# Performance work log

Measured on AMD Instinct MI355X. Metric: run time of the kernel, lower is better.

The kernel has to match this reference:

```python
import jax, jax.numpy as jnp
import numpy as np

N = 50000      # nodes
E = 800000     # edges
F = 128        # node feature dim (= output_size, residual)
H = 128        # hidden_size

def _uniform_fan_avg(key, shape):
    # VarianceScaling(scale=1.0, mode='fan_avg', distribution='uniform')
    fan_avg = (shape[0] + shape[1]) / 2.0
    limit = np.sqrt(3.0 / fan_avg)
    return jax.random.uniform(key, shape, jnp.float32, -limit, limit)

def setup_inputs() -> dict:
    key = jax.random.key(0)
    ks = jax.random.split(key, 16)
    h = jax.random.normal(ks[0], (N, F), jnp.float32)
    pos = jax.random.normal(ks[1], (N, 3), jnp.float32)
    senders = jax.random.randint(ks[2], (E,), 0, N, jnp.int32)
    receivers = jax.random.randint(ks[3], (E,), 0, N, jnp.int32)
    # edge_mlp: Linear(2F+1 -> H) silu, Linear(H -> H) silu (activate_final=True)
    eW1 = _uniform_fan_avg(ks[4], (2 * F + 1, H)); eb1 = jnp.zeros((H,), jnp.float32)
    eW2 = _uniform_fan_avg(ks[5], (H, H)); eb2 = jnp.zeros((H,), jnp.float32)
    # node_mlp: Linear(F+H -> H) silu, Linear(H -> F) (no final act)
    nW1 = _uniform_fan_avg(ks[6], (F + H, H)); nb1 = jnp.zeros((H,), jnp.float32)
    nW2 = _uniform_fan_avg(ks[7], (H, F)); nb2 = jnp.zeros((F,), jnp.float32)
    # pos_correction_mlp: Linear(H -> H) silu, Linear(H -> 1, no bias, UniformScaling(dt))
    pW1 = _uniform_fan_avg(ks[8], (H, H)); pb1 = jnp.zeros((H,), jnp.float32)
    dt = 0.001
    pW2 = jax.random.uniform(ks[9], (H, 1), jnp.float32, -dt, dt) * np.sqrt(3.0)
    return {"h": h, "pos": pos, "senders": senders, "receivers": receivers,
            "eW1": eW1, "eb1": eb1, "eW2": eW2, "eb2": eb2,
            "nW1": nW1, "nb1": nb1, "nW2": nW2, "nb2": nb2,
            "pW1": pW1, "pb1": pb1, "pW2": pW2}

def reference(h, pos, senders, receivers,
              eW1, eb1, eW2, eb2,
              nW1, nb1, nW2, nb2,
              pW1, pb1, pW2):
    n = h.shape[0]
    # _coord2radial (normalize=False)
    coord_diff = pos[senders] - pos[receivers]            # [E,3]
    radial = jnp.sum(coord_diff ** 2, axis=1, keepdims=True)  # [E,1]
    # edge update (_message): concat(h[senders], h[receivers], radial) -> edge_mlp
    msg_in = jnp.concatenate([h[senders], h[receivers], radial], axis=-1)  # [E,2F+1]
    msg = jax.nn.silu(msg_in @ eW1 + eb1)
    msg = jax.nn.silu(msg @ eW2 + eb2)                    # [E,H]
    # node update (_update): aggregate messages at receivers, node_mlp, residual
    agg = jax.ops.segment_sum(msg, receivers, num_segments=n)  # [N,H]
    x = jnp.concatenate([h, agg], axis=-1)                # [N,F+H]
    x = jax.nn.silu(x @ nW1 + nb1)
    x = x @ nW2 + nb2                                     # [N,F]
    h_new = h + x                                         # residual
    # position update (_pos_update)
    pc = jax.nn.silu(msg @ pW1 + pb1) @ pW2               # [E,1]
    trans = jnp.clip(coord_diff * pc, -100, 100)          # [E,3]
    pos_new = pos + jax.ops.segment_sum(trans, senders, num_segments=n)
    return h_new, pos_new
```

## Files before the change

### kernel.cpp

```cpp
#include <hip/hip_runtime.h>
#include <hip/hip_bf16.h>

#define NNODES 50000
#define NEDGES 800000
#define EB 1024
#define SCAN_BLOCKS 196
#define TRN_BLOCKS 448

typedef short bf16x8 __attribute__((ext_vector_type(8)));
typedef float f32x4 __attribute__((ext_vector_type(4)));
typedef unsigned short u16;
typedef unsigned int u32;

__device__ __forceinline__ u16 f2bf(float f) {
    __hip_bfloat16 b = __float2bfloat16(f);
    return *reinterpret_cast<u16*>(&b);
}
__device__ __forceinline__ float bf2f(u16 v) {
    u32 u = ((u32)v) << 16;
    return __uint_as_float(u);
}
__device__ __forceinline__ u32 pack2(float a, float b) {
    __hip_bfloat162 t = __float22bfloat162_rn(float2{a, b});
    return *reinterpret_cast<u32*>(&t);
}
__device__ __forceinline__ float fast_silu(float x) {
    float e = __builtin_amdgcn_exp2f(-1.442695040888963f * x);
    return x * __builtin_amdgcn_rcpf(1.0f + e);
}
__device__ __forceinline__ bf16x8 ld8(const u16* p) {
    return *(const bf16x8*)p;
}
__device__ __forceinline__ f32x4 mfma16(bf16x8 a, bf16x8 b, f32x4 c) {
    return __builtin_amdgcn_mfma_f32_16x16x32_bf16(a, b, c, 0, 0, 0);
}

__global__ void prep_kernel(const float* __restrict__ eW1, const float* __restrict__ eW2,
                            const float* __restrict__ pW1, const float* __restrict__ nW1,
                            const float* __restrict__ nW2,
                            u16* __restrict__ eW1T, u16* __restrict__ eW2T,
                            u16* __restrict__ pW1T, u16* __restrict__ nW1T,
                            u16* __restrict__ nW2T,
                            const int* __restrict__ rcv, int* __restrict__ counts) {
    int b = blockIdx.x;
    if (b < TRN_BLOCKS) {
        int i = b * 256 + threadIdx.x;
        const float* src; u16* dst; int K;
        if (i < 32768)      { src = eW1; dst = eW1T; K = 256; }
        else if (i < 49152) { src = eW2; dst = eW2T; K = 128; i -= 32768; }
        else if (i < 65536) { src = pW1; dst = pW1T; K = 128; i -= 49152; }
        else if (i < 98304) { src = nW1; dst = nW1T; K = 256; i -= 65536; }
        else                { src = nW2; dst = nW2T; K = 128; i -= 98304; }
        int n = i / K, k = i - n * K;
        dst[i] = f2bf(src[k * 128 + n]);
    } else {
        int e = (b - TRN_BLOCKS) * 256 + threadIdx.x;
        if (e < NEDGES) atomicAdd(&counts[rcv[e]], 1);
    }
}

__global__ __launch_bounds__(256) void gemm_p(
    const float* __restrict__ h, const u16* __restrict__ eW1T,
    const u16* __restrict__ nW1T, const float* __restrict__ eb1,
    u16* __restrict__ P)
{
    const int tid  = threadIdx.x;
    const int w    = tid >> 6;
    const int lane = tid & 63;
    const int m    = lane & 15;
    const int quad = lane >> 4;
    const int ksub = quad * 8;

    bf16x8 bw[4][6];
    float bias[6];
    #pragma unroll
    for (int cc = 0; cc < 6; cc++) {
        int C = 96 * w + 16 * cc + m;
        const u16* bp;
        if (C < 128)      { bp = eW1T + C * 256;               bias[cc] = 0.5f * eb1[C]; }
        else if (C < 256) { bp = eW1T + (C - 128) * 256 + 128; bias[cc] = 0.5f * eb1[C - 128]; }
        else              { bp = nW1T + (C - 256) * 256;       bias[cc] = 0.f; }
        #pragma unroll
        for (int t = 0; t < 4; t++) bw[t][cc] = ld8(bp + t * 32 + ksub);
    }
    const int base = blockIdx.x * 64;
    #pragma unroll
    for (int mt = 0; mt < 4; mt++) {
        int nm = base + mt * 16 + m;
        if (nm >= NNODES) nm = NNODES - 1;
        bf16x8 afr[4];
        #pragma unroll
        for (int t = 0; t < 4; t++) {
            const float* ap = h + (size_t)nm * 128 + t * 32 + ksub;
            f32x4 lo = *(const f32x4*)ap;
            f32x4 hi = *(const f32x4*)(ap + 4);
            #pragma unroll
            for (int j = 0; j < 4; j++) {
                afr[t][j]     = (short)f2bf(lo[j]);
                afr[t][4 + j] = (short)f2bf(hi[j]);
            }
        }
        f32x4 acc[6];
        #pragma unroll
        for (int cc = 0; cc < 6; cc++) acc[cc] = (f32x4){0,0,0,0};
        #pragma unroll
        for (int t = 0; t < 4; t++)
            #pragma unroll
            for (int cc = 0; cc < 6; cc++)
                acc[cc] = mfma16(afr[t], bw[t][cc], acc[cc]);
        #pragma unroll
        for (int cc = 0; cc < 6; cc++) {
            int C = 96 * w + 16 * cc + m;
            #pragma unroll
            for (int r = 0; r < 4; r++) {
                int nr = base + mt * 16 + quad * 4 + r;
                if (nr < NNODES) P[(size_t)nr * 384 + C] = f2bf(acc[cc][r] + bias[cc]);
            }
        }
    }
}

__global__ void scan1(const int* __restrict__ counts, int* __restrict__ excl,
                      int* __restrict__ blkSum) {
    __shared__ int tmp[256];
    int tx = threadIdx.x;
    int i = blockIdx.x * 256 + tx;
    int v = (i < NNODES) ? counts[i] : 0;
    tmp[tx] = v;
    __syncthreads();
    for (int off = 1; off < 256; off <<= 1) {
        int t = (tx >= off) ? tmp[tx - off] : 0;
        __syncthreads();
        tmp[tx] += t;
        __syncthreads();
    }
    if (i < NNODES) excl[i] = tmp[tx] - v;
    if (tx == 255) blkSum[blockIdx.x] = tmp[255];
}
__global__ void scan2(const int* __restrict__ blkSum, int* __restrict__ blkOff) {
    __shared__ int tmp[256];
    int tx = threadIdx.x;
    int v = (tx < SCAN_BLOCKS) ? blkSum[tx] : 0;
    tmp[tx] = v;
    __syncthreads();
    for (int off = 1; off < 256; off <<= 1) {
        int t = (tx >= off) ? tmp[tx - off] : 0;
        __syncthreads();
        tmp[tx] += t;
        __syncthreads();
    }
    if (tx < SCAN_BLOCKS) blkOff[tx] = tmp[tx] - v;
}
__global__ void scan3(const int* __restrict__ excl, const int* __restrict__ blkOff,
                      int* __restrict__ cursor) {
    int i = blockIdx.x * 256 + threadIdx.x;
    if (i < NNODES) cursor[i] = excl[i] + blkOff[blockIdx.x];
}
__global__ void scatter_kernel(const int* __restrict__ rcv, int* __restrict__ cursor,
                               int* __restrict__ perm) {
    int e = blockIdx.x * 256 + threadIdx.x;
    if (e < NEDGES) {
        int p = atomicAdd(&cursor[rcv[e]], 1);
        perm[p] = e;
    }
}

struct __align__(16) EdgeLds {
    u16   m1[64 * 136];
    u16   msg[64 * 136];
    float diff[64][4];
    float pcpart[4][64];
    float wlast[128];
    float radial[64];
    int   sndloc[64];
    int   rcvloc[64];
};

__global__ __launch_bounds__(256, 4) void edge_kernel(
    const u16* __restrict__ P, const float* __restrict__ pos,
    const int* __restrict__ snd, const int* __restrict__ rcv,
    const int* __restrict__ perm,
    const float* __restrict__ eW1last,
    const u16* __restrict__ eW2T, const float* __restrict__ eb2,
    const u16* __restrict__ pW1T, const float* __restrict__ pb1,
    const float* __restrict__ pW2,
    float* __restrict__ agg, float* __restrict__ posacc)
{
    __shared__ EdgeLds S;
    const int tid  = threadIdx.x;
    const int w    = tid >> 6;
    const int lane = tid & 63;
    const int m    = lane & 15;
    const int quad = lane >> 4;
    const int ksub = quad * 8;

    bf16x8 bw2[4][2], bp1[4][2];
    float b2v[2], pb1v[2], pw2v[2];
    #pragma unroll
    for (int cc = 0; cc < 2; cc++) {
        int col = (2 * w + cc) * 16 + m;
        #pragma unroll
        for (int t = 0; t < 4; t++) {
            bw2[t][cc] = ld8(eW2T + col * 128 + t * 32 + ksub);
            bp1[t][cc] = ld8(pW1T + col * 128 + t * 32 + ksub);
        }
        b2v[cc]  = eb2[col];
        pb1v[cc] = pb1[col];
        pw2v[cc] = pW2[col];
    }
    if (tid < 128) S.wlast[tid] = eW1last[tid];

    for (int base = blockIdx.x * 64; base < NEDGES; base += gridDim.x * 64) {
        __syncthreads();
        const int e = lane;
        int eg = perm[base + e];
        int s = snd[eg], r = rcv[eg];
        if (tid < 64) {
            S.sndloc[tid] = s; S.rcvloc[tid] = r;
            float rad = 0.f;
            #pragma unroll
            for (int c = 0; c < 3; c++) {
                float d = pos[s * 3 + c] - pos[r * 3 + c];
                S.diff[tid][c] = d;
                rad += d * d;
            }
            S.radial[tid] = rad;
        }
        __syncthreads();
        {
            float rad = S.radial[e];
            const u16* pa = P + (size_t)s * 384 + w * 32;
            const u16* pb = P + (size_t)r * 384 + 128 + w * 32;
            const int sw = e >> 3;
            #pragma unroll
            for (int k = 0; k < 4; k++) {
                bf16x8 va = ld8(pa + k * 8);
                bf16x8 vb = ld8(pb + k * 8);
                u32 pk[4];
                #pragma unroll
                for (int jj = 0; jj < 4; jj++) {
                    int col = w * 32 + k * 8 + jj * 2;
                    float2 wl = *(const float2*)&S.wlast[col];
                    float v0 = bf2f((u16)va[jj * 2])     + bf2f((u16)vb[jj * 2])     + rad * wl.x;
                    float v1 = bf2f((u16)va[jj * 2 + 1]) + bf2f((u16)vb[jj * 2 + 1]) + rad * wl.y;
                    pk[jj] = pack2(fast_silu(v0), fast_silu(v1));
                }
                int chunk = (w * 4 + k) ^ sw;
                *(uint4*)&S.m1[e * 136 + chunk * 8] =
                    make_uint4(pk[0], pk[1], pk[2], pk[3]);
            }
        }
        __syncthreads();
        #pragma unroll
        for (int mt = 0; mt < 4; mt++) {
            const int rs = mt * 2 + (m >> 3);
            const int row = mt * 16 + m;
            f32x4 acc0 = (f32x4){0,0,0,0}, acc1 = (f32x4){0,0,0,0};
            #pragma unroll
            for (int t = 0; t < 4; t++) {
                bf16x8 a = *(const bf16x8*)&S.m1[row * 136 + ((t * 4 + quad) ^ rs) * 8];
                acc0 = mfma16(a, bw2[t][0], acc0);
                acc1 = mfma16(a, bw2[t][1], acc1);
            }
            #pragma unroll
            for (int cc = 0; cc < 2; cc++) {
                f32x4 acc = cc ? acc1 : acc0;
                int col = (2 * w + cc) * 16 + m;
                #pragma unroll
                for (int rr = 0; rr < 4; rr++) {
                    int orow = mt * 16 + quad * 4 + rr;
                    S.msg[orow * 136 + col] = f2bf(fast_silu(acc[rr] + b2v[cc]));
                }
            }
        }
        __syncthreads();
        #pragma unroll
        for (int mt = 0; mt < 4; mt++) {
            f32x4 acc0 = (f32x4){0,0,0,0}, acc1 = (f32x4){0,0,0,0};
            #pragma unroll
            for (int t = 0; t < 4; t++) {
                bf16x8 a = *(const bf16x8*)&S.msg[(mt * 16 + m) * 136 + t * 32 + ksub];
                acc0 = mfma16(a, bp1[t][0], acc0);
                acc1 = mfma16(a, bp1[t][1], acc1);
            }
            float p4[4];
            #pragma unroll
            for (int rr = 0; rr < 4; rr++)
                p4[rr] = fast_silu(acc0[rr] + pb1v[0]) * pw2v[0]
                       + fast_silu(acc1[rr] + pb1v[1]) * pw2v[1];
            #pragma unroll
            for (int mask = 1; mask < 16; mask <<= 1) {
                #pragma unroll
                for (int rr = 0; rr < 4; rr++) p4[rr] += __shfl_xor(p4[rr], mask);
            }
            if (m == 0) {
                #pragma unroll
                for (int rr = 0; rr < 4; rr++)
                    S.pcpart[w][mt * 16 + quad * 4 + rr] = p4[rr];
            }
        }
        {
            int half = tid >> 7, col = tid & 127;
            int r0 = half * 32;
            float a = 0.f;
            int cur = S.rcvloc[r0];
            for (int rr = r0; rr < r0 + 32; ++rr) {
                int rc = S.rcvloc[rr];
                if (rc != cur) {
                    atomicAdd(&agg[(size_t)cur * 128 + col], a);
                    a = 0.f; cur = rc;
                }
                a += bf2f(S.msg[rr * 136 + col]);
            }
            atomicAdd(&agg[(size_t)cur * 128 + col], a);
        }
        __syncthreads();
        if (tid < 192) {
            int ee = tid / 3, c = tid - ee * 3;
            float pc = S.pcpart[0][ee] + S.pcpart[1][ee] + S.pcpart[2][ee] + S.pcpart[3][ee];
            float tr = S.diff[ee][c] * pc;
            tr = fminf(fmaxf(tr, -100.f), 100.f);
            atomicAdd(&posacc[S.sndloc[ee] * 3 + c], tr);
        }
    }
}

__global__ __launch_bounds__(256, 4) void node_kernel(
    const u16* __restrict__ P, const float* __restrict__ h,
    const float* __restrict__ agg,
    const u16* __restrict__ nW1T, const float* __restrict__ nb1,
    const u16* __restrict__ nW2T, const float* __restrict__ nb2,
    const float* __restrict__ pos, const float* __restrict__ posacc,
    float* __restrict__ out)
{
    __shared__ alignas(16) u16 m1[64 * 136];
    const int tid  = threadIdx.x;
    const int w    = tid >> 6;
    const int lane = tid & 63;
    const int m    = lane & 15;
    const int quad = lane >> 4;
    const int ksub = quad * 8;

    bf16x8 bw1[4][2], bw2[4][2];
    float b1v[2], b2v[2];
    #pragma unroll
    for (int cc = 0; cc < 2; cc++) {
        int col = (2 * w + cc) * 16 + m;
        #pragma unroll
        for (int t = 0; t < 4; t++) {
            bw1[t][cc] = ld8(nW1T + col * 256 + 128 + t * 32 + ksub);
            bw2[t][cc] = ld8(nW2T + col * 128 + t * 32 + ksub);
        }
        b1v[cc] = nb1[col];
        b2v[cc] = nb2[col];
    }
    const int base = blockIdx.x * 64;
    #pragma unroll
    for (int mt = 0; mt < 4; mt++) {
        int nm = base + mt * 16 + m;
        if (nm >= NNODES) nm = NNODES - 1;
        f32x4 acc0 = (f32x4){0,0,0,0}, acc1 = (f32x4){0,0,0,0};
        #pragma unroll
        for (int t = 0; t < 4; t++) {
            const float* ap = agg + (size_t)nm * 128 + t * 32 + ksub;
            f32x4 lo = *(const f32x4*)ap;
            f32x4 hi = *(const f32x4*)(ap + 4);
            bf16x8 a;
            #pragma unroll
            for (int j = 0; j < 4; j++) {
                a[j]     = (short)f2bf(lo[j]);
                a[4 + j] = (short)f2bf(hi[j]);
            }
            acc0 = mfma16(a, bw1[t][0], acc0);
            acc1 = mfma16(a, bw1[t][1], acc1);
        }
        #pragma unroll
        for (int cc = 0; cc < 2; cc++) {
            f32x4 acc = cc ? acc1 : acc0;
            int col = (2 * w + cc) * 16 + m;
            #pragma unroll
            for (int rr = 0; rr < 4; rr++) {
                int row = mt * 16 + quad * 4 + rr;
                int nrc = base + row; if (nrc >= NNODES) nrc = NNODES - 1;
                float v = acc[rr] + bf2f(P[(size_t)nrc * 384 + 256 + col]) + b1v[cc];
                m1[row * 136 + col] = f2bf(fast_silu(v));
            }
        }
    }
    __syncthreads();
    #pragma unroll
    for (int mt = 0; mt < 4; mt++) {
        f32x4 acc0 = (f32x4){0,0,0,0}, acc1 = (f32x4){0,0,0,0};
        #pragma unroll
        for (int t = 0; t < 4; t++) {
            bf16x8 a = *(const bf16x8*)&m1[(mt * 16 + m) * 136 + t * 32 + ksub];
            acc0 = mfma16(a, bw2[t][0], acc0);
            acc1 = mfma16(a, bw2[t][1], acc1);
        }
        #pragma unroll
        for (int cc = 0; cc < 2; cc++) {
            f32x4 acc = cc ? acc1 : acc0;
            int col = (2 * w + cc) * 16 + m;
            #pragma unroll
            for (int rr = 0; rr < 4; rr++) {
                int nr = base + mt * 16 + quad * 4 + rr;
                if (nr < NNODES)
                    out[(size_t)nr * 128 + col] = acc[rr] + b2v[cc] + h[(size_t)nr * 128 + col];
            }
        }
    }
    if (tid < 192) {
        int i = blockIdx.x * 192 + tid;
        if (i < NNODES * 3) out[NNODES * 128 + i] = pos[i] + posacc[i];
    }
}

extern "C" void kernel_launch(void* const* d_in, const int* in_sizes, int n_in,
                              void* d_out, int out_size, void* d_ws, size_t ws_size,
                              hipStream_t stream) {
    (void)in_sizes; (void)n_in; (void)out_size; (void)ws_size;
    const float* h   = (const float*)d_in[0];
    const float* pos = (const float*)d_in[1];
    const int*   snd = (const int*)d_in[2];
    const int*   rcv = (const int*)d_in[3];
    const float* eW1 = (const float*)d_in[4];
    const float* eb1 = (const float*)d_in[5];
    const float* eW2 = (const float*)d_in[6];
    const float* eb2 = (const float*)d_in[7];
    const float* nW1 = (const float*)d_in[8];
    const float* nb1 = (const float*)d_in[9];
    const float* nW2 = (const float*)d_in[10];
    const float* nb2 = (const float*)d_in[11];
    const float* pW1 = (const float*)d_in[12];
    const float* pb1 = (const float*)d_in[13];
    const float* pW2 = (const float*)d_in[14];
    float* out = (float*)d_out;

    float* agg    = (float*)d_ws;
    float* posacc = agg + (size_t)NNODES * 128;
    u16* P    = (u16*)(posacc + (size_t)NNODES * 3);
    u16* eW1T = P + (size_t)NNODES * 384;
    u16* eW2T = eW1T + 128 * 256;
    u16* pW1T = eW2T + 128 * 128;
    u16* nW1T = pW1T + 128 * 128;
    u16* nW2T = nW1T + 128 * 256;
    int* counts = (int*)(nW2T + 128 * 128);
    int* excl   = counts + 50048;
    int* blkSum = excl + 50048;
    int* blkOff = blkSum + 256;
    int* cursor = blkOff + 256;
    int* perm   = cursor + 50048;

    hipMemsetAsync(agg, 0, (size_t)NNODES * 131 * sizeof(float), stream);
    hipMemsetAsync(counts, 0, 50048 * sizeof(int), stream);

    prep_kernel<<<TRN_BLOCKS + (NEDGES + 255) / 256, 256, 0, stream>>>(
        eW1, eW2, pW1, nW1, nW2, eW1T, eW2T, pW1T, nW1T, nW2T, rcv, counts);

    gemm_p<<<(NNODES + 63) / 64, 256, 0, stream>>>(h, eW1T, nW1T, eb1, P);

    scan1<<<SCAN_BLOCKS, 256, 0, stream>>>(counts, excl, blkSum);
    scan2<<<1, 256, 0, stream>>>(blkSum, blkOff);
    scan3<<<SCAN_BLOCKS, 256, 0, stream>>>(excl, blkOff, cursor);
    scatter_kernel<<<(NEDGES + 255) / 256, 256, 0, stream>>>(rcv, cursor, perm);

    edge_kernel<<<EB, 256, 0, stream>>>(
        P, pos, snd, rcv, perm,
        eW1 + 256 * 128,
        eW2T, eb2, pW1T, pb1, pW2,
        agg, posacc);

    node_kernel<<<(NNODES + 63) / 64, 256, 0, stream>>>(
        P, h, agg, nW1T, nb1, nW2T, nb2, pos, posacc, out);
}
```

Before: 445.2 us.

## Software-pipeline edge gathers across iterations and use ballot bitmap for segment boundaries

Edge indices, positions and projected node features for the next 64-edge tile are prefetched into registers while the current tile's MFMA stages run, hiding gather latency. One block barrier is removed by computing the radial term in registers, and the others become lightweight LDS-only barriers. Segment boundaries for the receiver-sorted aggregation come from a wave ballot bitmap rather than a per-row compare loop. In exchange, register pressure rises under a 4-blocks-per-SIMD launch bound, which could cause spills. The custom barrier waits only on LDS counters, so it relies on global loads never being read through shared memory.

Measured after the change: 553.0 us. 1.24x slower.

```diff
diff --git a/kernel.cpp b/kernel.cpp
--- a/kernel.cpp
+++ b/kernel.cpp
@@ -33,6 +33,9 @@
 }
 __device__ __forceinline__ f32x4 mfma16(bf16x8 a, bf16x8 b, f32x4 c) {
     return __builtin_amdgcn_mfma_f32_16x16x32_bf16(a, b, c, 0, 0, 0);
+}
+__device__ __forceinline__ void bar_lds() {
+    asm volatile("s_waitcnt lgkmcnt(0)\n\ts_barrier" ::: "memory");
 }
 
 __global__ void prep_kernel(const float* __restrict__ eW1, const float* __restrict__ eW2,
@@ -171,9 +174,9 @@
     float diff[64][4];
     float pcpart[4][64];
     float wlast[128];
-    float radial[64];
     int   sndloc[64];
     int   rcvloc[64];
+    unsigned long long bmap;
 };
 
 __global__ __launch_bounds__(256, 4) void edge_kernel(
@@ -210,32 +213,53 @@
     }
     if (tid < 128) S.wlast[tid] = eW1last[tid];
 
-    for (int base = blockIdx.x * 64; base < NEDGES; base += gridDim.x * 64) {
-        __syncthreads();
-        const int e = lane;
-        int eg = perm[base + e];
-        int s = snd[eg], r = rcv[eg];
+    const int stride = gridDim.x * 64;
+
+    int s_n, r_n;
+    float ps_n[3], pr_n[3];
+    bf16x8 pa_n[4], pb_n[4];
+    {
+        int eg = perm[blockIdx.x * 64 + lane];
+        s_n = snd[eg]; r_n = rcv[eg];
+        #pragma unroll
+        for (int c = 0; c < 3; c++) { ps_n[c] = pos[s_n * 3 + c]; pr_n[c] = pos[r_n * 3 + c]; }
+        #pragma unroll
+        for (int t = 0; t < 4; t++) {
+            pa_n[t] = ld8(P + (size_t)s_n * 384 + w * 32 + t * 8);
+            pb_n[t] = ld8(P + (size_t)r_n * 384 + 128 + w * 32 + t * 8);
+        }
+    }
+
+    for (int base = blockIdx.x * 64; base < NEDGES; base += stride) {
+        int nbase = base + stride;
+        int pfb = (nbase < NEDGES) ? nbase : base;
+
+        bar_lds();
+        const int s = s_n, r = r_n;
+        const float d0 = ps_n[0] - pr_n[0];
+        const float d1 = ps_n[1] - pr_n[1];
+        const float d2 = ps_n[2] - pr_n[2];
+        const float rad = d0 * d0 + d1 * d1 + d2 * d2;
+        bf16x8 pa[4], pb[4];
+        #pragma unroll
+        for (int t = 0; t < 4; t++) { pa[t] = pa_n[t]; pb[t] = pb_n[t]; }
+
+        int eg_n = perm[pfb + lane];
+
         if (tid < 64) {
             S.sndloc[tid] = s; S.rcvloc[tid] = r;
-            float rad = 0.f;
-            #pragma unroll
-            for (int c = 0; c < 3; c++) {
-                float d = pos[s * 3 + c] - pos[r * 3 + c];
-                S.diff[tid][c] = d;
-                rad += d * d;
-            }
-            S.radial[tid] = rad;
-        }
-        __syncthreads();
+            S.diff[tid][0] = d0; S.diff[tid][1] = d1; S.diff[tid][2] = d2;
+            int pv = __shfl_up(r, 1);
+            unsigned long long bm = __ballot(lane > 0 && r != pv);
+            if (tid == 0) S.bmap = bm;
+        }
+
         {
-            float rad = S.radial[e];
-            const u16* pa = P + (size_t)s * 384 + w * 32;
-            const u16* pb = P + (size_t)r * 384 + 128 + w * 32;
-            const int sw = e >> 3;
+            const int sw = lane >> 3;
             #pragma unroll
             for (int k = 0; k < 4; k++) {
-                bf16x8 va = ld8(pa + k * 8);
-                bf16x8 vb = ld8(pb + k * 8);
+                bf16x8 va = pa[k];
+                bf16x8 vb = pb[k];
                 u32 pk[4];
                 #pragma unroll
                 for (int jj = 0; jj < 4; jj++) {
@@ -246,11 +270,14 @@
                     pk[jj] = pack2(fast_silu(v0), fast_silu(v1));
                 }
                 int chunk = (w * 4 + k) ^ sw;
-                *(uint4*)&S.m1[e * 136 + chunk * 8] =
+                *(uint4*)&S.m1[lane * 136 + chunk * 8] =
                     make_uint4(pk[0], pk[1], pk[2], pk[3]);
             }
         }
-        __syncthreads();
+
+        s_n = snd[eg_n]; r_n = rcv[eg_n];
+
+        bar_lds();
         #pragma unroll
         for (int mt = 0; mt < 4; mt++) {
             const int rs = mt * 2 + (m >> 3);
@@ -273,7 +300,16 @@
                 }
             }
         }
-        __syncthreads();
+
+        #pragma unroll
+        for (int c = 0; c < 3; c++) { ps_n[c] = pos[s_n * 3 + c]; pr_n[c] = pos[r_n * 3 + c]; }
+        #pragma unroll
+        for (int t = 0; t < 4; t++) {
+            pa_n[t] = ld8(P + (size_t)s_n * 384 + w * 32 + t * 8);
+            pb_n[t] = ld8(P + (size_t)r_n * 384 + 128 + w * 32 + t * 8);
+        }
+
+        bar_lds();
         #pragma unroll
         for (int mt = 0; mt < 4; mt++) {
             f32x4 acc0 = (f32x4){0,0,0,0}, acc1 = (f32x4){0,0,0,0};
@@ -302,19 +338,22 @@
         {
             int half = tid >> 7, col = tid & 127;
             int r0 = half * 32;
+            u32 bm32 = __builtin_amdgcn_readfirstlane((u32)(S.bmap >> r0)) & ~1u;
             float a = 0.f;
             int cur = S.rcvloc[r0];
-            for (int rr = r0; rr < r0 + 32; ++rr) {
-                int rc = S.rcvloc[rr];
-                if (rc != cur) {
-                    atomicAdd(&agg[(size_t)cur * 128 + col], a);
-                    a = 0.f; cur = rc;
-                }
-                a += bf2f(S.msg[rr * 136 + col]);
-            }
-            atomicAdd(&agg[(size_t)cur * 128 + col], a);
-        }
-        __syncthreads();
+            int rr = r0;
+            const int end0 = r0 + 32;
+            while (true) {
+                int nb = bm32 ? (r0 + __builtin_ctz(bm32)) : end0;
+                for (; rr < nb; ++rr) a += bf2f(S.msg[rr * 136 + col]);
+                atomicAdd(&agg[(size_t)cur * 128 + col], a);
+                if (nb == end0) break;
+                a = 0.f;
+                cur = S.rcvloc[nb];
+                bm32 &= bm32 - 1;
+            }
+        }
+        bar_lds();
         if (tid < 192) {
             int ee = tid / 3, c = tid - ee * 3;
             float pc = S.pcpart[0][ee] + S.pcpart[1][ee] + S.pcpart[2][ee] + S.pcpart[3][ee];
```
